# Optimization experiments

Hardware: AMD Instinct MI355X
Metric: run time of the kernel (lower is better)

Reference implementation:

```python
import jax, jax.numpy as jnp
import numpy as np

N_NODES = 50000
N_EDGES = 800000
NODE_DIM = 256
EDGE_DIM = 64
NUM_REL = 4
HID = 512      # hidden_dims[0]
LAST = 128     # last_dim_size
BATCH = 16384
EPS = 1e-10    # torchdrug RelationalGraphConv degree-normalization eps


def _glorot(k, shape):
    fan_in = shape[-1]
    return jax.random.normal(k, shape, jnp.float32) / np.sqrt(fan_in).astype(np.float32)


def setup_inputs() -> dict:
    key = jax.random.key(0)
    ks = jax.random.split(key, 20)
    inp = {}
    inp["inputs"] = jax.random.randint(ks[0], (BATCH, 3), 0, N_NODES, dtype=jnp.int32)
    inp["node_feature"] = jax.random.normal(ks[1], (N_NODES, NODE_DIM), jnp.float32)
    inp["edge_feature"] = jax.random.normal(ks[2], (N_EDGES, EDGE_DIM), jnp.float32)
    inp["edge_src"] = jax.random.randint(ks[3], (N_EDGES,), 0, N_NODES, dtype=jnp.int32)
    inp["edge_dst"] = jax.random.randint(ks[4], (N_EDGES,), 0, N_NODES, dtype=jnp.int32)
    inp["edge_rel"] = jax.random.randint(ks[5], (N_EDGES,), 0, NUM_REL, dtype=jnp.int32)
    # RGCN layer 1: 256 -> 512
    inp["We1"] = _glorot(ks[6], (NODE_DIM, EDGE_DIM)); inp["be1"] = jnp.zeros((NODE_DIM,), jnp.float32)
    inp["Wl1"] = _glorot(ks[7], (HID, NUM_REL * NODE_DIM)); inp["bl1"] = jnp.zeros((HID,), jnp.float32)
    inp["Ws1"] = _glorot(ks[8], (HID, NODE_DIM)); inp["bs1"] = jnp.zeros((HID,), jnp.float32)
    # RGCN layer 2: 512 -> 128
    inp["We2"] = _glorot(ks[9], (HID, EDGE_DIM)); inp["be2"] = jnp.zeros((HID,), jnp.float32)
    inp["Wl2"] = _glorot(ks[10], (LAST, NUM_REL * HID)); inp["bl2"] = jnp.zeros((LAST,), jnp.float32)
    inp["Ws2"] = _glorot(ks[11], (LAST, HID)); inp["bs2"] = jnp.zeros((LAST,), jnp.float32)
    # ccle_mlp: edge_dim -> 256 -> 128
    inp["Wc1"] = _glorot(ks[12], (256, EDGE_DIM)); inp["bc1"] = jnp.zeros((256,), jnp.float32)
    inp["Wc2"] = _glorot(ks[13], (LAST, 256)); inp["bc2"] = jnp.zeros((LAST,), jnp.float32)
    # final MLP: 3*128 -> 128 -> 64 -> 1
    inp["Wf1"] = _glorot(ks[14], (128, 3 * LAST)); inp["bf1"] = jnp.zeros((128,), jnp.float32)
    inp["Wf2"] = _glorot(ks[15], (64, 128)); inp["bf2"] = jnp.zeros((64,), jnp.float32)
    inp["Wf3"] = _glorot(ks[16], (1, 64)); inp["bf3"] = jnp.zeros((1,), jnp.float32)
    return inp


def _rgcn_layer(x, edge_src, edge_dst, edge_rel, edge_feat, We, be, Wl, bl, Ws, bs):
    """torchdrug RelationalGraphConv: message = x[src] + edge_linear(edge_feat);
    per-(node,relation) mean aggregation; combine = linear(update) + self_loop(x); relu."""
    in_dim = x.shape[1]
    msg = x[edge_src] + edge_feat @ We.T + be                      # [E, in_dim]
    seg = edge_dst * NUM_REL + edge_rel                            # [E]
    agg = jax.ops.segment_sum(msg, seg, num_segments=N_NODES * NUM_REL)
    cnt = jax.ops.segment_sum(jnp.ones((msg.shape[0], 1), msg.dtype), seg,
                              num_segments=N_NODES * NUM_REL)
    upd = (agg / (cnt + EPS)).reshape(N_NODES, NUM_REL * in_dim)   # [N, R*in_dim]
    return jax.nn.relu(upd @ Wl.T + bl + x @ Ws.T + bs)


def reference(inputs, node_feature, edge_feature, edge_src, edge_dst, edge_rel,
              We1, be1, Wl1, bl1, Ws1, bs1,
              We2, be2, Wl2, bl2, Ws2, bs2,
              Wc1, bc1, Wc2, bc2,
              Wf1, bf1, Wf2, bf2, Wf3, bf3):
    d1, d2, ctx = inputs[:, 0], inputs[:, 1], inputs[:, 2]
    h = _rgcn_layer(node_feature, edge_src, edge_dst, edge_rel, edge_feature,
                    We1, be1, Wl1, bl1, Ws1, bs1)
    h = _rgcn_layer(h, edge_src, edge_dst, edge_rel, edge_feature,
                    We2, be2, Wl2, bl2, Ws2, bs2)
    x1 = h[d1]                                                     # [B, 128]
    x2 = h[d2]                                                     # [B, 128]
    ef = edge_feature[ctx]                                         # [B, 64]
    x3 = jax.nn.relu(ef @ Wc1.T + bc1) @ Wc2.T + bc2               # [B, 128]
    x = jnp.concatenate([x1, x2, x3], axis=1)                      # [B, 384]
    x = jax.nn.relu(x @ Wf1.T + bf1)
    x = jax.nn.relu(x @ Wf2.T + bf2)
    return x @ Wf3.T + bf3                                         # [B, 1]
```

## Files before the change

### kernel.cpp

```cpp
#include <hip/hip_runtime.h>
#include <hip/hip_bf16.h>

#define N_NODES 50000
#define N_EDGES 800000
#define NODE_DIM 256
#define EDGE_DIM 64
#define NUM_REL 4
#define HID 512
#define LAST 128
#define BATCH 16384
#define EPS 1e-10f
#define NSEG (N_NODES * NUM_REL)

#define K1 1568
#define K2 800

typedef __bf16 bf16_t;
typedef __attribute__((ext_vector_type(8))) __bf16 bf16x8;
typedef __attribute__((ext_vector_type(4))) __bf16 bf16x4;
typedef __attribute__((ext_vector_type(2))) __bf16 bf16x2;
typedef __attribute__((ext_vector_type(4))) float f32x4;

typedef __attribute__((address_space(1))) const unsigned int g_u32;
typedef __attribute__((address_space(3))) unsigned int l_u32;
static __device__ __forceinline__ void gload16(const void* g, void* l) {
    __builtin_amdgcn_global_load_lds((g_u32*)g, (l_u32*)l, 16, 0, 0);
}

__global__ __launch_bounds__(256) void hist_kernel(
    const int* __restrict__ edst, const int* __restrict__ erel, int* __restrict__ hist)
{
    int e = blockIdx.x * 256 + threadIdx.x;
    if (e >= N_EDGES) return;
    atomicAdd(&hist[edst[e] * NUM_REL + erel[e]], 1);
}

#define SCAN_B 2048
__global__ __launch_bounds__(256) void scan1(
    const int* __restrict__ in, int* __restrict__ out, int* __restrict__ bsum, int n)
{
    __shared__ int sh[256];
    int base = blockIdx.x * SCAN_B + threadIdx.x * 8;
    int v[8]; int s = 0;
#pragma unroll
    for (int i = 0; i < 8; ++i) {
        int idx = base + i;
        v[i] = s;
        s += (idx < n) ? in[idx] : 0;
    }
    sh[threadIdx.x] = s;
    __syncthreads();
    for (int off = 1; off < 256; off <<= 1) {
        int t = (threadIdx.x >= off) ? sh[threadIdx.x - off] : 0;
        __syncthreads();
        sh[threadIdx.x] += t;
        __syncthreads();
    }
    int texcl = (threadIdx.x == 0) ? 0 : sh[threadIdx.x - 1];
#pragma unroll
    for (int i = 0; i < 8; ++i) {
        int idx = base + i;
        if (idx < n) out[idx] = texcl + v[i];
    }
    if (threadIdx.x == 255) bsum[blockIdx.x] = sh[255];
}

__global__ void scan2(int* bsum, int nb)
{
    if (threadIdx.x == 0 && blockIdx.x == 0) {
        int s = 0;
        for (int i = 0; i < nb; ++i) { int t = bsum[i]; bsum[i] = s; s += t; }
    }
}

__global__ __launch_bounds__(256) void scan3(int* __restrict__ out, const int* __restrict__ bsum, int n)
{
    int idx = blockIdx.x * SCAN_B + threadIdx.x * 8;
    int add = bsum[blockIdx.x];
#pragma unroll
    for (int i = 0; i < 8; ++i)
        if (idx + i < n) out[idx + i] += add;
}

__global__ __launch_bounds__(256) void csr_fill(
    const int* __restrict__ edst, const int* __restrict__ erel, const int* __restrict__ esrc,
    const int* __restrict__ offs, int* __restrict__ cursor,
    int* __restrict__ csr_src, int* __restrict__ csr_eid)
{
    int e = blockIdx.x * 256 + threadIdx.x;
    if (e >= N_EDGES) return;
    int seg = edst[e] * NUM_REL + erel[e];
    int pos = offs[seg] + atomicAdd(&cursor[seg], 1);
    csr_src[pos] = esrc[e];
    csr_eid[pos] = e;
}

__global__ __launch_bounds__(256) void f2bf4_k(const float* __restrict__ src, bf16_t* __restrict__ dst, int n4)
{
    int i = blockIdx.x * 256 + threadIdx.x;
    if (i >= n4) return;
    float4 v = ((const float4*)src)[i];
    bf16x4 o;
    o[0] = (bf16_t)v.x; o[1] = (bf16_t)v.y; o[2] = (bf16_t)v.z; o[3] = (bf16_t)v.w;
    ((bf16x4*)dst)[i] = o;
}

__global__ __launch_bounds__(256) void addbias_k(const float* __restrict__ a, const float* __restrict__ b,
                                                 float* __restrict__ o, int n)
{
    int i = blockIdx.x * 256 + threadIdx.x;
    if (i < n) o[i] = a[i] + b[i];
}

__global__ __launch_bounds__(256) void xconv_k(const float* __restrict__ x, bf16_t* __restrict__ A1,
                                               bf16_t* __restrict__ xb)
{
    int i = blockIdx.x * 256 + threadIdx.x;
    int n = i >> 6;
    int c4 = i & 63;
    float4 v = ((const float4*)(x + (size_t)n * 256))[c4];
    bf16x4 o;
    o[0] = (bf16_t)v.x; o[1] = (bf16_t)v.y; o[2] = (bf16_t)v.z; o[3] = (bf16_t)v.w;
    *(bf16x4*)(A1 + (size_t)n * K1 + 1280 + c4 * 4) = o;
    *(bf16x4*)(xb + (size_t)n * 256 + c4 * 4) = o;
}

__global__ __launch_bounds__(256) void prep_w1cat(
    const float* __restrict__ Wl1, const float* __restrict__ We1,
    const float* __restrict__ Ws1, const float* __restrict__ be1, bf16_t* __restrict__ W1cat)
{
    int j = blockIdx.x;
    int t = threadIdx.x;
    const float* wrow = Wl1 + (size_t)j * 1024;
    bf16_t* out = W1cat + (size_t)j * K1;
    for (int c = t; c < 1024; c += 256) out[c] = (bf16_t)wrow[c];
    {
        int r = t >> 6, e = t & 63;
        float s = 0.f;
        const float* wr = wrow + r * 256;
        for (int c = 0; c < 256; ++c) s += wr[c] * We1[c * 64 + e];
        out[1024 + t] = (bf16_t)s;
    }
    if (t < 256) out[1280 + t] = (bf16_t)Ws1[(size_t)j * 256 + t];
    if (t < 4) {
        float s = 0.f;
        const float* wr = wrow + t * 256;
        for (int c = 0; c < 256; ++c) s += wr[c] * be1[c];
        out[1536 + t] = (bf16_t)s;
    }
    if (t >= 4 && t < 32) out[1536 + t] = (bf16_t)0.f;
}

__global__ __launch_bounds__(256) void prep_w2cat(
    const float* __restrict__ Wl2, const float* __restrict__ We2,
    const float* __restrict__ Ws2, const float* __restrict__ be2, bf16_t* __restrict__ W2cat)
{
    int j = blockIdx.x;
    int t = threadIdx.x;
    const float* wrow = Wl2 + (size_t)j * 2048;
    bf16_t* out = W2cat + (size_t)j * K2;
    {
        int r = t >> 6, e = t & 63;
        float s = 0.f;
        const float* wr = wrow + r * 512;
        for (int k = 0; k < 512; ++k) s += wr[k] * We2[k * 64 + e];
        out[t] = (bf16_t)s;
    }
    for (int c = t; c < 512; c += 256) out[256 + c] = (bf16_t)Ws2[(size_t)j * 512 + c];
    if (t < 4) {
        float s = 0.f;
        const float* wr = wrow + t * 512;
        for (int k = 0; k < 512; ++k) s += wr[k] * be2[k];
        out[768 + t] = (bf16_t)s;
    }
    if (t >= 4 && t < 32) out[768 + t] = (bf16_t)0.f;
}

__global__ __launch_bounds__(256) void prep_w2p(const float* __restrict__ Wl2, bf16_t* __restrict__ W2p)
{
    int idx = blockIdx.x * 256 + threadIdx.x;
    int row = idx >> 9, k = idx & 511;
    int j = row & 127, r = row >> 7;
    W2p[idx] = (bf16_t)Wl2[(size_t)j * 2048 + r * 512 + k];
}

__global__ __launch_bounds__(256) void agg1(
    const float* __restrict__ ef, const bf16_t* __restrict__ xb,
    const int* __restrict__ csr_src, const int* __restrict__ csr_eid,
    const int* __restrict__ offs, const int* __restrict__ hist,
    bf16_t* __restrict__ A1, bf16_t* __restrict__ A2)
{
    int n = blockIdx.x;
    int w = threadIdx.x >> 6;
    int lane = threadIdx.x & 63;
    int seg = n * NUM_REL + w;
    int beg = offs[seg], ct = hist[seg];
    float a0 = 0.f, a1 = 0.f, a2 = 0.f, a3 = 0.f, aef = 0.f;
    int i = 0;
    for (; i + 4 <= ct; i += 4) {
        int s0 = csr_src[beg + i], s1 = csr_src[beg + i + 1];
        int s2 = csr_src[beg + i + 2], s3 = csr_src[beg + i + 3];
        int e0 = csr_eid[beg + i], e1 = csr_eid[beg + i + 1];
        int e2 = csr_eid[beg + i + 2], e3 = csr_eid[beg + i + 3];
        bf16x4 v0 = *(const bf16x4*)(xb + (size_t)s0 * 256 + lane * 4);
        bf16x4 v1 = *(const bf16x4*)(xb + (size_t)s1 * 256 + lane * 4);
        bf16x4 v2 = *(const bf16x4*)(xb + (size_t)s2 * 256 + lane * 4);
        bf16x4 v3 = *(const bf16x4*)(xb + (size_t)s3 * 256 + lane * 4);
        float f0 = ef[(size_t)e0 * 64 + lane];
        float f1 = ef[(size_t)e1 * 64 + lane];
        float f2 = ef[(size_t)e2 * 64 + lane];
        float f3 = ef[(size_t)e3 * 64 + lane];
        a0 += (float)v0[0] + (float)v1[0] + (float)v2[0] + (float)v3[0];
        a1 += (float)v0[1] + (float)v1[1] + (float)v2[1] + (float)v3[1];
        a2 += (float)v0[2] + (float)v1[2] + (float)v2[2] + (float)v3[2];
        a3 += (float)v0[3] + (float)v1[3] + (float)v2[3] + (float)v3[3];
        aef += f0 + f1 + f2 + f3;
    }
    for (; i < ct; ++i) {
        int s0 = csr_src[beg + i];
        int e0 = csr_eid[beg + i];
        bf16x4 v0 = *(const bf16x4*)(xb + (size_t)s0 * 256 + lane * 4);
        a0 += (float)v0[0]; a1 += (float)v0[1]; a2 += (float)v0[2]; a3 += (float)v0[3];
        aef += ef[(size_t)e0 * 64 + lane];
    }
    float inv = 1.0f / ((float)ct + EPS);
    bf16x4 m;
    m[0] = (bf16_t)(a0 * inv); m[1] = (bf16_t)(a1 * inv);
    m[2] = (bf16_t)(a2 * inv); m[3] = (bf16_t)(a3 * inv);
    *(bf16x4*)(A1 + (size_t)n * K1 + w * 256 + lane * 4) = m;
    bf16_t ev = (bf16_t)(aef * inv);
    A1[(size_t)n * K1 + 1024 + w * 64 + lane] = ev;
    A2[(size_t)n * K2 + w * 64 + lane] = ev;
    if (lane == 0) {
        bf16_t fv = (bf16_t)((float)ct * inv);
        A1[(size_t)n * K1 + 1536 + w] = fv;
        A2[(size_t)n * K2 + 768 + w] = fv;
    }
    if (w == 3) {
        if (lane >= 4 && lane < 32)  A1[(size_t)n * K1 + 1536 + lane] = (bf16_t)0.f;
        if (lane >= 36 && lane < 64) A2[(size_t)n * K2 + 772 + (lane - 36)] = (bf16_t)0.f;
    }
}

__global__ __launch_bounds__(256) void agg2(
    const bf16_t* __restrict__ P, const int* __restrict__ csr_src,
    const int* __restrict__ offs, const int* __restrict__ hist,
    float* __restrict__ h2base)
{
    __shared__ float red[4][128];
    int n = blockIdx.x;
    int w = threadIdx.x >> 6;
    int lane = threadIdx.x & 63;
    int seg = n * NUM_REL + w;
    int beg = offs[seg], ct = hist[seg];
    float s0 = 0.f, s1 = 0.f;
    int i = 0;
    for (; i + 4 <= ct; i += 4) {
        int a = csr_src[beg + i], b = csr_src[beg + i + 1];
        int c = csr_src[beg + i + 2], d = csr_src[beg + i + 3];
        bf16x2 va = *(const bf16x2*)(P + (size_t)a * HID + w * 128 + lane * 2);
        bf16x2 vb = *(const bf16x2*)(P + (size_t)b * HID + w * 128 + lane * 2);
        bf16x2 vc = *(const bf16x2*)(P + (size_t)c * HID + w * 128 + lane * 2);
        bf16x2 vd = *(const bf16x2*)(P + (size_t)d * HID + w * 128 + lane * 2);
        s0 += (float)va[0] + (float)vb[0] + (float)vc[0] + (float)vd[0];
        s1 += (float)va[1] + (float)vb[1] + (float)vc[1] + (float)vd[1];
    }
    for (; i < ct; ++i) {
        int a = csr_src[beg + i];
        bf16x2 va = *(const bf16x2*)(P + (size_t)a * HID + w * 128 + lane * 2);
        s0 += (float)va[0]; s1 += (float)va[1];
    }
    float inv = 1.0f / ((float)ct + EPS);
    red[w][lane * 2] = s0 * inv;
    red[w][lane * 2 + 1] = s1 * inv;
    __syncthreads();
    int t = threadIdx.x;
    if (t < 128)
        h2base[(size_t)n * 128 + t] = red[0][t] + red[1][t] + red[2][t] + red[3][t];
}

template<int RELU, int ACC, int OUTBF>
__global__ __launch_bounds__(256) void gemm_bf16(
    const bf16_t* __restrict__ A, int lda,
    const bf16_t* __restrict__ W, int ldw,
    const float* __restrict__ Cin, int ldcin,
    const float* __restrict__ bias,
    void* __restrict__ Cout, int ldc,
    int M, int N, int K)
{
    __shared__ char smem[16384];
    char* As = smem;
    char* Bs = smem + 8192;
    const int tid = threadIdx.x;
    const int row0 = blockIdx.x * 128;
    const int col0 = blockIdx.y * 128;
    const int lane = tid & 63, wv = tid >> 6;

    const int srow = wv * 32 + (lane >> 2);
    const int schunk = (lane & 3) * 8;
    int ga0 = row0 + srow;      if (ga0 >= M) ga0 = M - 1;
    int ga1 = row0 + srow + 16; if (ga1 >= M) ga1 = M - 1;
    int gb0 = col0 + srow;      if (gb0 >= N) gb0 = N - 1;
    int gb1 = col0 + srow + 16; if (gb1 >= N) gb1 = N - 1;
    const bf16_t* pa0 = A + (size_t)ga0 * lda + schunk;
    const bf16_t* pa1 = A + (size_t)ga1 * lda + schunk;
    const bf16_t* pb0 = W + (size_t)gb0 * ldw + schunk;
    const bf16_t* pb1 = W + (size_t)gb1 * ldw + schunk;
    char* lA0 = As + wv * 2048;
    char* lA1 = As + wv * 2048 + 1024;
    char* lB0 = Bs + wv * 2048;
    char* lB1 = Bs + wv * 2048 + 1024;

    const int wm = wv >> 1, wn = wv & 1;
    const int r16 = lane & 15, kch = lane >> 4;

    f32x4 zero = {0.f, 0.f, 0.f, 0.f};
    f32x4 acc[4][4];
#pragma unroll
    for (int i = 0; i < 4; ++i)
#pragma unroll
        for (int j = 0; j < 4; ++j) acc[i][j] = zero;

    for (int k0 = 0; k0 < K; k0 += 32) {
        gload16(pa0 + k0, lA0);
        gload16(pa1 + k0, lA1);
        gload16(pb0 + k0, lB0);
        gload16(pb1 + k0, lB1);
        __syncthreads();
        bf16x8 af[4], bfm[4];
#pragma unroll
        for (int i = 0; i < 4; ++i)
            af[i] = *(const bf16x8*)(As + (wm * 64 + i * 16 + r16) * 64 + kch * 16);
#pragma unroll
        for (int j = 0; j < 4; ++j)
            bfm[j] = *(const bf16x8*)(Bs + (wn * 64 + j * 16 + r16) * 64 + kch * 16);
#pragma unroll
        for (int i = 0; i < 4; ++i)
#pragma unroll
            for (int j = 0; j < 4; ++j)
                acc[i][j] = __builtin_amdgcn_mfma_f32_16x16x32_bf16(af[i], bfm[j], acc[i][j], 0, 0, 0);
        __syncthreads();
    }

    const int crow0 = row0 + wm * 64;
#pragma unroll
    for (int i = 0; i < 4; ++i) {
#pragma unroll
        for (int j = 0; j < 4; ++j) {
            int col = col0 + wn * 64 + j * 16 + r16;
            if (col >= N) continue;
            float bv = bias ? bias[col] : 0.f;
#pragma unroll
            for (int q = 0; q < 4; ++q) {
                int row = crow0 + i * 16 + kch * 4 + q;
                if (row >= M) continue;
                float v = acc[i][j][q] + bv;
                if (ACC) v += Cin[(size_t)row * ldcin + col];
                if (RELU) v = fmaxf(v, 0.f);
                if (OUTBF) ((bf16_t*)Cout)[(size_t)row * ldc + col] = (bf16_t)v;
                else       ((float*)Cout)[(size_t)row * ldc + col] = v;
            }
        }
    }
}

__global__ __launch_bounds__(256) void gather_head(
    const int* __restrict__ inputs, const bf16_t* __restrict__ h2,
    const float* __restrict__ ef, bf16_t* __restrict__ xcat, bf16_t* __restrict__ ef_g)
{
    int i = blockIdx.x;
    int t = threadIdx.x;
    int d1 = inputs[i * 3 + 0];
    int d2 = inputs[i * 3 + 1];
    int ctx = inputs[i * 3 + 2];
    if (t < 128) {
        xcat[(size_t)i * 384 + t] = h2[(size_t)d1 * LAST + t];
    } else {
        int c = t - 128;
        xcat[(size_t)i * 384 + 128 + c] = h2[(size_t)d2 * LAST + c];
    }
    if (t < 64) ef_g[(size_t)i * 64 + t] = (bf16_t)ef[(size_t)ctx * EDGE_DIM + t];
}

__global__ __launch_bounds__(256) void final_matvec(
    const bf16_t* __restrict__ f2, const float* __restrict__ Wf3,
    const float* __restrict__ bf3, float* __restrict__ out, int M)
{
    int row = blockIdx.x * 4 + (threadIdx.x >> 6);
    int lane = threadIdx.x & 63;
    if (row >= M) return;
    float v = (float)f2[(size_t)row * 64 + lane] * Wf3[lane];
#pragma unroll
    for (int off = 32; off > 0; off >>= 1) v += __shfl_down(v, off);
    if (lane == 0) out[row] = v + bf3[0];
}

extern "C" void kernel_launch(void* const* d_in, const int* in_sizes, int n_in,
                              void* d_out, int out_size, void* d_ws, size_t ws_size,
                              hipStream_t stream)
{
    const int*   inputs       = (const int*)  d_in[0];
    const float* node_feature = (const float*)d_in[1];
    const float* edge_feature = (const float*)d_in[2];
    const int*   edge_src     = (const int*)  d_in[3];
    const int*   edge_dst     = (const int*)  d_in[4];
    const int*   edge_rel     = (const int*)  d_in[5];
    const float* We1 = (const float*)d_in[6];
    const float* be1 = (const float*)d_in[7];
    const float* Wl1 = (const float*)d_in[8];
    const float* bl1 = (const float*)d_in[9];
    const float* Ws1 = (const float*)d_in[10];
    const float* bs1 = (const float*)d_in[11];
    const float* We2 = (const float*)d_in[12];
    const float* be2 = (const float*)d_in[13];
    const float* Wl2 = (const float*)d_in[14];
    const float* bl2 = (const float*)d_in[15];
    const float* Ws2 = (const float*)d_in[16];
    const float* bs2 = (const float*)d_in[17];
    const float* Wc1 = (const float*)d_in[18];
    const float* bc1 = (const float*)d_in[19];
    const float* Wc2 = (const float*)d_in[20];
    const float* bc2 = (const float*)d_in[21];
    const float* Wf1 = (const float*)d_in[22];
    const float* bf1 = (const float*)d_in[23];
    const float* Wf2 = (const float*)d_in[24];
    const float* bf2 = (const float*)d_in[25];
    const float* Wf3 = (const float*)d_in[26];
    const float* bf3 = (const float*)d_in[27];
    float* out = (float*)d_out;

    char* p = (char*)d_ws;
    auto alloc = [&](size_t bytes) { char* r = p; p += (bytes + 255) & ~(size_t)255; return r; };
    int* hist     = (int*)alloc(NSEG * 4);
    int* offs     = (int*)alloc(NSEG * 4);
    int* cursor   = (int*)alloc(NSEG * 4);
    int* csr_src  = (int*)alloc(N_EDGES * 4);
    int* csr_eid  = (int*)alloc(N_EDGES * 4);
    int* bsums    = (int*)alloc(128 * 4);
    bf16_t* A1    = (bf16_t*)alloc((size_t)N_NODES * K1 * 2);
    bf16_t* A2    = (bf16_t*)alloc((size_t)N_NODES * K2 * 2);
    bf16_t* xb    = (bf16_t*)alloc((size_t)N_NODES * 256 * 2);
    bf16_t* Pbuf  = (bf16_t*)alloc((size_t)N_NODES * HID * 2);
    float*  h2base= (float*)alloc((size_t)N_NODES * 128 * 4);
    bf16_t* h2    = (bf16_t*)alloc((size_t)N_NODES * 128 * 2);
    bf16_t* W1cat = (bf16_t*)alloc((size_t)512 * K1 * 2);
    bf16_t* W2cat = (bf16_t*)alloc((size_t)128 * K2 * 2);
    bf16_t* W2p   = (bf16_t*)alloc((size_t)512 * 512 * 2);
    bf16_t* Wc1b  = (bf16_t*)alloc(256 * 64 * 2);
    bf16_t* Wc2b  = (bf16_t*)alloc(128 * 256 * 2);
    bf16_t* Wf1b  = (bf16_t*)alloc(128 * 384 * 2);
    bf16_t* Wf2b  = (bf16_t*)alloc(64 * 128 * 2);
    float*  bias12= (float*)alloc(512 * 4);
    float*  bias22= (float*)alloc(128 * 4);
    bf16_t* ef_g  = (bf16_t*)alloc((size_t)BATCH * 64 * 2);
    bf16_t* u3    = (bf16_t*)alloc((size_t)BATCH * 256 * 2);
    bf16_t* xcat  = (bf16_t*)alloc((size_t)BATCH * 384 * 2);
    bf16_t* f1    = (bf16_t*)alloc((size_t)BATCH * 128 * 2);
    bf16_t* f2    = (bf16_t*)alloc((size_t)BATCH * 64 * 2);

    hipMemsetAsync(hist, 0, NSEG * 4, stream);
    hipMemsetAsync(cursor, 0, NSEG * 4, stream);
    hist_kernel<<<(N_EDGES + 255) / 256, 256, 0, stream>>>(edge_dst, edge_rel, hist);
    int nscan = (NSEG + SCAN_B - 1) / SCAN_B;
    scan1<<<nscan, 256, 0, stream>>>(hist, offs, bsums, NSEG);
    scan2<<<1, 64, 0, stream>>>(bsums, nscan);
    scan3<<<nscan, 256, 0, stream>>>(offs, bsums, NSEG);
    csr_fill<<<(N_EDGES + 255) / 256, 256, 0, stream>>>(edge_dst, edge_rel, edge_src,
                                                        offs, cursor, csr_src, csr_eid);

    prep_w1cat<<<512, 256, 0, stream>>>(Wl1, We1, Ws1, be1, W1cat);
    prep_w2cat<<<128, 256, 0, stream>>>(Wl2, We2, Ws2, be2, W2cat);
    prep_w2p<<<(512 * 512) / 256, 256, 0, stream>>>(Wl2, W2p);
    f2bf4_k<<<(256 * 64 / 4 + 255) / 256, 256, 0, stream>>>(Wc1, Wc1b, 256 * 64 / 4);
    f2bf4_k<<<(128 * 256 / 4 + 255) / 256, 256, 0, stream>>>(Wc2, Wc2b, 128 * 256 / 4);
    f2bf4_k<<<(128 * 384 / 4 + 255) / 256, 256, 0, stream>>>(Wf1, Wf1b, 128 * 384 / 4);
    f2bf4_k<<<(64 * 128 / 4 + 255) / 256, 256, 0, stream>>>(Wf2, Wf2b, 64 * 128 / 4);
    addbias_k<<<2, 256, 0, stream>>>(bl1, bs1, bias12, 512);
    addbias_k<<<1, 256, 0, stream>>>(bl2, bs2, bias22, 128);
    xconv_k<<<(N_NODES * 64 + 255) / 256, 256, 0, stream>>>(node_feature, A1, xb);

    agg1<<<N_NODES, 256, 0, stream>>>(edge_feature, xb, csr_src, csr_eid, offs, hist, A1, A2);
    {
        dim3 g((N_NODES + 127) / 128, HID / 128);
        gemm_bf16<1, 0, 1><<<g, 256, 0, stream>>>(A1, K1, W1cat, K1, nullptr, 0, bias12,
                                                  A2 + 256, K2, N_NODES, HID, K1);
    }

    {
        dim3 g((N_NODES + 127) / 128, HID / 128);
        gemm_bf16<0, 0, 1><<<g, 256, 0, stream>>>(A2 + 256, K2, W2p, 512, nullptr, 0, nullptr,
                                                  Pbuf, HID, N_NODES, HID, HID);
    }
    agg2<<<N_NODES, 256, 0, stream>>>(Pbuf, csr_src, offs, hist, h2base);
    {
        dim3 g((N_NODES + 127) / 128, 1);
        gemm_bf16<1, 1, 1><<<g, 256, 0, stream>>>(A2, K2, W2cat, K2, h2base, 128, bias22,
                                                  h2, 128, N_NODES, 128, K2);
    }

    gather_head<<<BATCH, 256, 0, stream>>>(inputs, h2, edge_feature, xcat, ef_g);
    {
        dim3 g(BATCH / 128, 2);
        gemm_bf16<1, 0, 1><<<g, 256, 0, stream>>>(ef_g, 64, Wc1b, 64, nullptr, 0, bc1,
                                                  u3, 256, BATCH, 256, 64);
    }
    {
        dim3 g(BATCH / 128, 1);
        gemm_bf16<0, 0, 1><<<g, 256, 0, stream>>>(u3, 256, Wc2b, 256, nullptr, 0, bc2,
                                                  xcat + 256, 384, BATCH, 128, 256);
    }
    {
        dim3 g(BATCH / 128, 1);
        gemm_bf16<1, 0, 1><<<g, 256, 0, stream>>>(xcat, 384, Wf1b, 384, nullptr, 0, bf1,
                                                  f1, 128, BATCH, 128, 384);
    }
    {
        dim3 g(BATCH / 128, 1);
        gemm_bf16<1, 0, 1><<<g, 256, 0, stream>>>(f1, 128, Wf2b, 128, nullptr, 0, bf2,
                                                  f2, 64, BATCH, 64, 128);
    }
    final_matvec<<<BATCH / 4, 256, 0, stream>>>(f2, Wf3, bf3, out, BATCH);
}
```

Baseline: 821.2 us.

## Double GEMM K-tile to 64 with XOR-swizzled LDS and column-fastest block order

The bf16 MFMA GEMM now loads a 64-wide K slice per iteration into a 32KB LDS tile, and uses an XOR swizzle on the 16-byte chunks to avoid LDS bank conflicts. This halves the number of barrier pairs per K. The grid is flattened to 1D with column tiles fastest, so blocks sharing the same A rows run close together and reuse them in cache. K1/K2 padding grows to multiples of 64, which requires zero-filling more padding columns in the weights and activations. The cost is more LDS per block, which may lower occupancy.

```diff
diff --git a/kernel.cpp b/kernel.cpp
--- a/kernel.cpp
+++ b/kernel.cpp
@@ -12,8 +12,8 @@
 #define EPS 1e-10f
 #define NSEG (N_NODES * NUM_REL)
 
-#define K1 1568
-#define K2 800
+#define K1 1600
+#define K2 832
 
 typedef __bf16 bf16_t;
 typedef __attribute__((ext_vector_type(8))) __bf16 bf16x8;
@@ -148,7 +148,7 @@
         for (int c = 0; c < 256; ++c) s += wr[c] * be1[c];
         out[1536 + t] = (bf16_t)s;
     }
-    if (t >= 4 && t < 32) out[1536 + t] = (bf16_t)0.f;
+    if (t >= 4 && t < 64) out[1536 + t] = (bf16_t)0.f;
 }
 
 __global__ __launch_bounds__(256) void prep_w2cat(
@@ -173,7 +173,7 @@
         for (int k = 0; k < 512; ++k) s += wr[k] * be2[k];
         out[768 + t] = (bf16_t)s;
     }
-    if (t >= 4 && t < 32) out[768 + t] = (bf16_t)0.f;
+    if (t >= 4 && t < 64) out[768 + t] = (bf16_t)0.f;
 }
 
 __global__ __launch_bounds__(256) void prep_w2p(const float* __restrict__ Wl2, bf16_t* __restrict__ W2p)
@@ -236,9 +236,9 @@
         A1[(size_t)n * K1 + 1536 + w] = fv;
         A2[(size_t)n * K2 + 768 + w] = fv;
     }
-    if (w == 3) {
-        if (lane >= 4 && lane < 32)  A1[(size_t)n * K1 + 1536 + lane] = (bf16_t)0.f;
-        if (lane >= 36 && lane < 64) A2[(size_t)n * K2 + 772 + (lane - 36)] = (bf16_t)0.f;
+    if (w == 3 && lane >= 4) {
+        A1[(size_t)n * K1 + 1536 + lane] = (bf16_t)0.f;
+        A2[(size_t)n * K2 + 768 + lane] = (bf16_t)0.f;
     }
 }
 
@@ -286,33 +286,34 @@
     const float* __restrict__ Cin, int ldcin,
     const float* __restrict__ bias,
     void* __restrict__ Cout, int ldc,
-    int M, int N, int K)
-{
-    __shared__ char smem[16384];
+    int M, int N, int K, int ncol)
+{
+    __shared__ char smem[32768];
     char* As = smem;
-    char* Bs = smem + 8192;
+    char* Bs = smem + 16384;
     const int tid = threadIdx.x;
-    const int row0 = blockIdx.x * 128;
-    const int col0 = blockIdx.y * 128;
+    const int row0 = (blockIdx.x / ncol) * 128;
+    const int col0 = (blockIdx.x % ncol) * 128;
     const int lane = tid & 63, wv = tid >> 6;
 
-    const int srow = wv * 32 + (lane >> 2);
-    const int schunk = (lane & 3) * 8;
-    int ga0 = row0 + srow;      if (ga0 >= M) ga0 = M - 1;
-    int ga1 = row0 + srow + 16; if (ga1 >= M) ga1 = M - 1;
-    int gb0 = col0 + srow;      if (gb0 >= N) gb0 = N - 1;
-    int gb1 = col0 + srow + 16; if (gb1 >= N) gb1 = N - 1;
-    const bf16_t* pa0 = A + (size_t)ga0 * lda + schunk;
-    const bf16_t* pa1 = A + (size_t)ga1 * lda + schunk;
-    const bf16_t* pb0 = W + (size_t)gb0 * ldw + schunk;
-    const bf16_t* pb1 = W + (size_t)gb1 * ldw + schunk;
-    char* lA0 = As + wv * 2048;
-    char* lA1 = As + wv * 2048 + 1024;
-    char* lB0 = Bs + wv * 2048;
-    char* lB1 = Bs + wv * 2048 + 1024;
+    const int rsub = lane >> 3;
+    const int gchunk = (lane & 7) ^ rsub;
+    const bf16_t* pa[4]; const bf16_t* pb[4];
+    char* la[4]; char* lb[4];
+#pragma unroll
+    for (int s = 0; s < 4; ++s) {
+        int q = wv * 4 + s;
+        int ar = row0 + q * 8 + rsub; if (ar >= M) ar = M - 1;
+        int br = col0 + q * 8 + rsub; if (br >= N) br = N - 1;
+        pa[s] = A + (size_t)ar * lda + gchunk * 8;
+        pb[s] = W + (size_t)br * ldw + gchunk * 8;
+        la[s] = As + q * 1024;
+        lb[s] = Bs + q * 1024;
+    }
 
     const int wm = wv >> 1, wn = wv & 1;
     const int r16 = lane & 15, kch = lane >> 4;
+    const int sw = r16 & 7;
 
     f32x4 zero = {0.f, 0.f, 0.f, 0.f};
     f32x4 acc[4][4];
@@ -321,24 +322,29 @@
 #pragma unroll
         for (int j = 0; j < 4; ++j) acc[i][j] = zero;
 
-    for (int k0 = 0; k0 < K; k0 += 32) {
-        gload16(pa0 + k0, lA0);
-        gload16(pa1 + k0, lA1);
-        gload16(pb0 + k0, lB0);
-        gload16(pb1 + k0, lB1);
+    for (int k0 = 0; k0 < K; k0 += 64) {
+#pragma unroll
+        for (int s = 0; s < 4; ++s) {
+            gload16(pa[s] + k0, la[s]);
+            gload16(pb[s] + k0, lb[s]);
+        }
         __syncthreads();
-        bf16x8 af[4], bfm[4];
-#pragma unroll
-        for (int i = 0; i < 4; ++i)
-            af[i] = *(const bf16x8*)(As + (wm * 64 + i * 16 + r16) * 64 + kch * 16);
-#pragma unroll
-        for (int j = 0; j < 4; ++j)
-            bfm[j] = *(const bf16x8*)(Bs + (wn * 64 + j * 16 + r16) * 64 + kch * 16);
-#pragma unroll
-        for (int i = 0; i < 4; ++i)
+#pragma unroll
+        for (int t = 0; t < 2; ++t) {
+            const int slot = ((t * 4 + kch) ^ sw) << 4;
+            bf16x8 af[4], bfm[4];
+#pragma unroll
+            for (int i = 0; i < 4; ++i)
+                af[i] = *(const bf16x8*)(As + (wm * 64 + i * 16 + r16) * 128 + slot);
 #pragma unroll
             for (int j = 0; j < 4; ++j)
-                acc[i][j] = __builtin_amdgcn_mfma_f32_16x16x32_bf16(af[i], bfm[j], acc[i][j], 0, 0, 0);
+                bfm[j] = *(const bf16x8*)(Bs + (wn * 64 + j * 16 + r16) * 128 + slot);
+#pragma unroll
+            for (int i = 0; i < 4; ++i)
+#pragma unroll
+                for (int j = 0; j < 4; ++j)
+                    acc[i][j] = __builtin_amdgcn_mfma_f32_16x16x32_bf16(af[i], bfm[j], acc[i][j], 0, 0, 0);
+        }
         __syncthreads();
     }
 
@@ -481,43 +487,39 @@
 
     agg1<<<N_NODES, 256, 0, stream>>>(edge_feature, xb, csr_src, csr_eid, offs, hist, A1, A2);
     {
-        dim3 g((N_NODES + 127) / 128, HID / 128);
-        gemm_bf16<1, 0, 1><<<g, 256, 0, stream>>>(A1, K1, W1cat, K1, nullptr, 0, bias12,
-                                                  A2 + 256, K2, N_NODES, HID, K1);
-    }
-
-    {
-        dim3 g((N_NODES + 127) / 128, HID / 128);
-        gemm_bf16<0, 0, 1><<<g, 256, 0, stream>>>(A2 + 256, K2, W2p, 512, nullptr, 0, nullptr,
-                                                  Pbuf, HID, N_NODES, HID, HID);
+        int nrow = (N_NODES + 127) / 128, ncol = HID / 128;
+        gemm_bf16<1, 0, 1><<<nrow * ncol, 256, 0, stream>>>(A1, K1, W1cat, K1, nullptr, 0, bias12,
+                                                            A2 + 256, K2, N_NODES, HID, K1, ncol);
+    }
+
+    {
+        int nrow = (N_NODES + 127) / 128, ncol = HID / 128;
+        gemm_bf16<0, 0, 1><<<nrow * ncol, 256, 0, stream>>>(A2 + 256, K2, W2p, 512, nullptr, 0, nullptr,
+                                                            Pbuf, HID, N_NODES, HID, 512, ncol);
     }
     agg2<<<N_NODES, 256, 0, stream>>>(Pbuf, csr_src, offs, hist, h2base);
     {
-        dim3 g((N_NODES + 127) / 128, 1);
-        gemm_bf16<1, 1, 1><<<g, 256, 0, stream>>>(A2, K2, W2cat, K2, h2base, 128, bias22,
-                                                  h2, 128, N_NODES, 128, K2);
+        int nrow = (N_NODES + 127) / 128;
+        gemm_bf16<1, 1, 1><<<nrow, 256, 0, stream>>>(A2, K2, W2cat, K2, h2base, 128, bias22,
+                                                     h2, 128, N_NODES, 128, K2, 1);
     }
 
     gather_head<<<BATCH, 256, 0, stream>>>(inputs, h2, edge_feature, xcat, ef_g);
     {
-        dim3 g(BATCH / 128, 2);
-        gemm_bf16<1, 0, 1><<<g, 256, 0, stream>>>(ef_g, 64, Wc1b, 64, nullptr, 0, bc1,
-                                                  u3, 256, BATCH, 256, 64);
-    }
-    {
-        dim3 g(BATCH / 128, 1);
-        gemm_bf16<0, 0, 1><<<g, 256, 0, stream>>>(u3, 256, Wc2b, 256, nullptr, 0, bc2,
-                                                  xcat + 256, 384, BATCH, 128, 256);
-    }
-    {
-        dim3 g(BATCH / 128, 1);
-        gemm_bf16<1, 0, 1><<<g, 256, 0, stream>>>(xcat, 384, Wf1b, 384, nullptr, 0, bf1,
-                                                  f1, 128, BATCH, 128, 384);
-    }
-    {
-        dim3 g(BATCH / 128, 1);
-        gemm_bf16<1, 0, 1><<<g, 256, 0, stream>>>(f1, 128, Wf2b, 128, nullptr, 0, bf2,
-                                                  f2, 64, BATCH, 64, 128);
+        gemm_bf16<1, 0, 1><<<(BATCH / 128) * 2, 256, 0, stream>>>(ef_g, 64, Wc1b, 64, nullptr, 0, bc1,
+                                                                  u3, 256, BATCH, 256, 64, 2);
+    }
+    {
+        gemm_bf16<0, 0, 1><<<BATCH / 128, 256, 0, stream>>>(u3, 256, Wc2b, 256, nullptr, 0, bc2,
+                                                            xcat + 256, 384, BATCH, 128, 256, 1);
+    }
+    {
+        gemm_bf16<1, 0, 1><<<BATCH / 128, 256, 0, stream>>>(xcat, 384, Wf1b, 384, nullptr, 0, bf1,
+                                                            f1, 128, BATCH, 128, 384, 1);
+    }
+    {
+        gemm_bf16<1, 0, 1><<<BATCH / 128, 256, 0, stream>>>(f1, 128, Wf2b, 128, nullptr, 0, bf2,
+                                                            f2, 64, BATCH, 64, 128, 1);
     }
     final_matvec<<<BATCH / 4, 256, 0, stream>>>(f2, Wf3, bf3, out, BATCH);
 }
```

Result: faster. 750.2 us (-8.6%).
